# Kernel optimization log

Hardware: AMD Instinct MI355X
Metric: run time of the kernel (lower is better)

The kernel has to match this reference:

```python
import jax, jax.numpy as jnp
import numpy as np

N_NODE = 100000
HIDDEN = 128
BATCH = 4096
SESS_LEN = 50


def setup_inputs() -> dict:
    key = jax.random.key(0)
    k1, k2, k3, k4, k5 = jax.random.split(key, 5)
    return {
        "item_embedding": jax.random.normal(k1, (N_NODE, HIDDEN), dtype=jnp.float32),
        "items": jax.random.randint(k2, (BATCH, SESS_LEN), 0, N_NODE, dtype=jnp.int64),
        "A": jax.random.uniform(k3, (BATCH, BATCH), dtype=jnp.float32),
        "D": jax.random.uniform(k4, (BATCH, BATCH), dtype=jnp.float32),
        "target_embedding": jax.random.normal(k5, (BATCH, 1, 2 * HIDDEN), dtype=jnp.float32),
    }


def reference(item_embedding, items, A, D, target_embedding):
    # Gather per-session item embeddings: (batch, sess_len, hidden)
    seq_h = item_embedding[items]
    # Sum over session positions -> (batch, hidden)
    relation_emb = jnp.sum(seq_h, axis=1)
    # DA = D @ A, then propagate: (batch, batch) @ (batch, hidden)
    DA = jnp.matmul(D, A)
    relation_emb = jnp.matmul(DA, relation_emb)
    # Row-wise L2 normalization (torch.norm(dim=-1))
    norm = jnp.linalg.norm(relation_emb, axis=-1, keepdims=True)
    return relation_emb / norm
```

## Files before the change

### kernel.cpp

```cpp
#include <hip/hip_runtime.h>
#include <hip/hip_bf16.h>

#define BATCH   4096
#define HIDDEN  128
#define SESS    50
#define KTOT    4096
#define NB      ((size_t)BATCH * HIDDEN)

typedef __bf16 bf16x8 __attribute__((ext_vector_type(8)));
typedef float  f32x4  __attribute__((ext_vector_type(4)));
typedef float  f32x2  __attribute__((ext_vector_type(2)));

__device__ __forceinline__ f32x4 mfma_bf16(bf16x8 a, bf16x8 b, f32x4 c) {
    return __builtin_amdgcn_mfma_f32_16x16x32_bf16(a, b, c, 0, 0, 0);
}

__device__ __forceinline__ void gload16(const void* g, void* l) {
    __builtin_amdgcn_global_load_lds(
        (const __attribute__((address_space(1))) void*)g,
        (__attribute__((address_space(3))) void*)l, 16, 0, 0);
}


__global__ __launch_bounds__(256)
void gather_sum_kernel(const float* __restrict__ emb,
                       const int* __restrict__ items32,
                       __bf16* __restrict__ ETp) {
    __shared__ int sidx[4][SESS];
    const int t  = threadIdx.x;
    const int b0 = blockIdx.x * 4;
    const bool is64 = (items32[1] | items32[3] | items32[5] | items32[7] |
                       items32[9] | items32[11] | items32[13] | items32[15]) == 0;
    if (t < 4 * SESS) {
        const int w_ = t / SESS, s_ = t % SESS;
        sidx[w_][s_] = is64
            ? (int)((const long long*)items32)[(long)(b0 + w_) * SESS + s_]
            : items32[(b0 + w_) * SESS + s_];
    }
    __syncthreads();
    const int w    = t >> 6;
    const int lane = t & 63;
    const int c    = lane & 31;
    const int h    = lane >> 5;
    f32x4 acc = {0.f, 0.f, 0.f, 0.f};
#pragma unroll
    for (int i = 0; i < 25; ++i) {
        acc += *(const f32x4*)(emb + (long)sidx[w][h + 2 * i] * HIDDEN + c * 4);
    }
#pragma unroll
    for (int j = 0; j < 4; ++j) acc[j] += __shfl_xor(acc[j], 32, 64);
    if (h == 0) {
        const int b  = b0 + w;
        const int h0 = c * 4;
        const long pb = ((long)(b >> 3) << 10) + (b & 7) + ((h0 >> 4) << 7);
#pragma unroll
        for (int j = 0; j < 4; ++j)
            ETp[pb + ((h0 & 15) + j) * 8] = (__bf16)acc[j];
    }
}

__global__ __launch_bounds__(256, 2)
void gemm_mfma_kernel(const float* __restrict__ X,
                      const __bf16* __restrict__ Bpk,
                      float* __restrict__ Tp) {
    __shared__ __align__(16) float raw[16384];
    const int tid  = threadIdx.x;
    const int wave = tid >> 6;
    const int lane = tid & 63;
    const int lo   = lane & 15;
    const int quad = lane >> 4;
    const int rowBase = blockIdx.x * 16;
    const int sy      = blockIdx.y;
    const int kBase   = sy * 1024 + wave * 256;

    const float* apt   = X + (long)(rowBase + lo) * KTOT + kBase + quad * 8;
    const char*  bsrc  = (const char*)Bpk + ((long)(kBase >> 3) << 11);
    char*        sbase = (char*)raw + wave * 16384;

    f32x4 acc[8];
#pragma unroll
    for (int i = 0; i < 8; ++i) acc[i] = (f32x4){0.f, 0.f, 0.f, 0.f};

    f32x4 xa0[2], xa1[2];

#define STAGE(ks_, cur_) do {                                                \
    const char* g_ = bsrc + (ks_) * 8192 + lane * 16;                        \
    char* l_ = sbase + (cur_) * 8192;                                        \
    _Pragma("unroll")                                                        \
    for (int i_ = 0; i_ < 8; ++i_)                                           \
        gload16(g_ + i_ * 1024, l_ + i_ * 1024);                             \
} while (0)

    xa0[0] = *(const f32x4*)(apt);
    xa1[0] = *(const f32x4*)(apt + 4);
    STAGE(0, 0);
    xa0[1] = *(const f32x4*)(apt + 32);
    xa1[1] = *(const f32x4*)(apt + 36);
    STAGE(1, 1);

#define GITER(ks_, cur_, WAIT_, PRE_) do {                                   \
    asm volatile(WAIT_ ::: "memory");                                        \
    bf16x8 bb[8];                                                            \
    _Pragma("unroll")                                                        \
    for (int nt_ = 0; nt_ < 8; ++nt_)                                        \
        bb[nt_] = *(const bf16x8*)(sbase + (cur_) * 8192 + quad * 2048 +     \
                                   nt_ * 256 + lo * 16);                     \
    bf16x8 a;                                                                \
    a[0] = (__bf16)xa0[cur_][0]; a[1] = (__bf16)xa0[cur_][1];                \
    a[2] = (__bf16)xa0[cur_][2]; a[3] = (__bf16)xa0[cur_][3];                \
    a[4] = (__bf16)xa1[cur_][0]; a[5] = (__bf16)xa1[cur_][1];                \
    a[6] = (__bf16)xa1[cur_][2]; a[7] = (__bf16)xa1[cur_][3];                \
    asm volatile("s_waitcnt lgkmcnt(0)" ::: "memory");                       \
    __builtin_amdgcn_sched_barrier(0);                                       \
    if (PRE_) {                                                              \
        xa0[cur_] = *(const f32x4*)(apt + ((ks_) + 2) * 32);                 \
        xa1[cur_] = *(const f32x4*)(apt + ((ks_) + 2) * 32 + 4);             \
        STAGE((ks_) + 2, cur_);                                              \
    }                                                                        \
    _Pragma("unroll")                                                        \
    for (int nt_ = 0; nt_ < 8; ++nt_)                                        \
        acc[nt_] = mfma_bf16(a, bb[nt_], acc[nt_]);                          \
} while (0)

    GITER(0, 0, "s_waitcnt vmcnt(10)", 1);
    GITER(1, 1, "s_waitcnt vmcnt(10)", 1);
    GITER(2, 0, "s_waitcnt vmcnt(10)", 1);
    GITER(3, 1, "s_waitcnt vmcnt(10)", 1);
    GITER(4, 0, "s_waitcnt vmcnt(10)", 1);
    GITER(5, 1, "s_waitcnt vmcnt(10)", 1);
    GITER(6, 0, "s_waitcnt vmcnt(10)", 0);
    GITER(7, 1, "s_waitcnt vmcnt(0)",  0);

#undef GITER
#undef STAGE

    __syncthreads();
    float (*red)[16][132] = (float (*)[16][132])raw;
#pragma unroll
    for (int r = 0; r < 4; ++r) {
        const int dr = quad * 4 + r;
#pragma unroll
        for (int nt = 0; nt < 8; ++nt)
            red[wave][dr][nt * 16 + lo] = acc[nt][r];
    }
    __syncthreads();
    const int row = tid >> 4;
    const int cb  = (tid & 15) * 8;
    f32x4 v0 = {0.f, 0.f, 0.f, 0.f}, v1 = {0.f, 0.f, 0.f, 0.f};
#pragma unroll
    for (int w = 0; w < 4; ++w) {
        v0 += *(const f32x4*)&red[w][row][cb];
        v1 += *(const f32x4*)&red[w][row][cb + 4];
    }
    float* outp = Tp + (size_t)sy * NB + (long)(rowBase + row) * HIDDEN + cb;
    *(f32x4*)(outp)     = v0;
    *(f32x4*)(outp + 4) = v1;
}

__global__ __launch_bounds__(256)
void reduce4_kernel(const float* __restrict__ Tp, __bf16* __restrict__ TTp) {
    const size_t i = ((size_t)blockIdx.x * 256 + threadIdx.x) * 4;
    f32x4 a = *(const f32x4*)(Tp + i);
    a += *(const f32x4*)(Tp + NB + i);
    a += *(const f32x4*)(Tp + 2 * NB + i);
    a += *(const f32x4*)(Tp + 3 * NB + i);
    const int b  = (int)(i >> 7);
    const int h0 = (int)(i & 127);
    const long pb = ((long)(b >> 3) << 10) + (b & 7) + ((h0 >> 4) << 7);
#pragma unroll
    for (int j = 0; j < 4; ++j)
        TTp[pb + ((h0 & 15) + j) * 8] = (__bf16)a[j];
}

__global__ __launch_bounds__(256)
void reduce_norm_kernel(const float* __restrict__ Tp, float* __restrict__ out) {
    const int t    = threadIdx.x;
    const int w    = t >> 6;
    const int lane = t & 63;
    const int row  = blockIdx.x * 4 + w;
    const size_t base = (size_t)row * HIDDEN + lane * 2;
    f32x2 v = *(const f32x2*)(Tp + base);
    v += *(const f32x2*)(Tp + NB + base);
    v += *(const f32x2*)(Tp + 2 * NB + base);
    v += *(const f32x2*)(Tp + 3 * NB + base);
    float sq = v[0] * v[0] + v[1] * v[1];
#pragma unroll
    for (int m = 1; m < 64; m <<= 1) sq += __shfl_xor(sq, m, 64);
    const float s = rsqrtf(sq);
    f32x2 o = {v[0] * s, v[1] * s};
    *(f32x2*)(out + base) = o;
}

extern "C" void kernel_launch(void* const* d_in, const int* in_sizes, int n_in,
                              void* d_out, int out_size, void* d_ws, size_t ws_size,
                              hipStream_t stream) {
    const float* emb   = (const float*)d_in[0];
    const int*   items = (const int*)d_in[1];
    const float* A     = (const float*)d_in[2];
    const float* D     = (const float*)d_in[3];
    float* out = (float*)d_out;

    __bf16* ETp = (__bf16*)d_ws;
    __bf16* TTp = ETp + NB;
    float*  Tp  = (float*)(TTp + NB);

    gather_sum_kernel<<<BATCH / 4, 256, 0, stream>>>(emb, items, ETp);

    gemm_mfma_kernel<<<dim3(BATCH / 16, 4), 256, 0, stream>>>(A, ETp, Tp);
    reduce4_kernel<<<512, 256, 0, stream>>>(Tp, TTp);

    gemm_mfma_kernel<<<dim3(BATCH / 16, 4), 256, 0, stream>>>(D, TTp, Tp);
    reduce_norm_kernel<<<BATCH / 4, 256, 0, stream>>>(Tp, out);
}
```

Measured before the change: 229.4 us.

## Drop split-K in GEMMs and fuse reductions and normalization into epilogues

The GEMM kernel stops splitting K across four blocks and partial-sum buffers. Each block now walks the full K range, staging the fp32 X tile through double-buffered LDS with global-to-LDS loads and streaming B directly from global memory, with the N dimension split across waves. The bf16 repack for the second GEMM and the row L2 normalization move into the GEMM epilogues, which removes two reduction kernels and the fp32 partial-sum round trips. In exchange there are four times fewer blocks (256 blocks, one per CU), so latency hiding and parallelism drop, and B is no longer shared through LDS.

```diff
diff --git a/kernel.cpp b/kernel.cpp
--- a/kernel.cpp
+++ b/kernel.cpp
@@ -7,9 +7,15 @@
 #define KTOT    4096
 #define NB      ((size_t)BATCH * HIDDEN)
 
+#define BK        512
+#define KCH       16
+#define NTILES    (KTOT / BK)
+#define ROWSTRIDE 2064
+#define BUFSZ     (16 * ROWSTRIDE)
+
 typedef __bf16 bf16x8 __attribute__((ext_vector_type(8)));
+typedef __bf16 bf16x4 __attribute__((ext_vector_type(4)));
 typedef float  f32x4  __attribute__((ext_vector_type(4)));
-typedef float  f32x2  __attribute__((ext_vector_type(2)));
 
 __device__ __forceinline__ f32x4 mfma_bf16(bf16x8 a, bf16x8 b, f32x4 c) {
     return __builtin_amdgcn_mfma_f32_16x16x32_bf16(a, b, c, 0, 0, 0);
@@ -59,136 +65,115 @@
     }
 }
 
-__global__ __launch_bounds__(256, 2)
+template <int PHASE>
+__global__ __launch_bounds__(256, 1)
 void gemm_mfma_kernel(const float* __restrict__ X,
                       const __bf16* __restrict__ Bpk,
-                      float* __restrict__ Tp) {
-    __shared__ __align__(16) float raw[16384];
+                      __bf16* __restrict__ TTp,
+                      float* __restrict__ out) {
+    __shared__ __align__(16) char lds[2 * BUFSZ];
     const int tid  = threadIdx.x;
-    const int wave = tid >> 6;
+    const int w    = tid >> 6;
     const int lane = tid & 63;
     const int lo   = lane & 15;
     const int quad = lane >> 4;
     const int rowBase = blockIdx.x * 16;
-    const int sy      = blockIdx.y;
-    const int kBase   = sy * 1024 + wave * 256;
 
-    const float* apt   = X + (long)(rowBase + lo) * KTOT + kBase + quad * 8;
-    const char*  bsrc  = (const char*)Bpk + ((long)(kBase >> 3) << 11);
-    char*        sbase = (char*)raw + wave * 16384;
+    const float* xb = X + (size_t)(rowBase + 4 * w) * KTOT + lane * 4;
 
-    f32x4 acc[8];
-#pragma unroll
-    for (int i = 0; i < 8; ++i) acc[i] = (f32x4){0.f, 0.f, 0.f, 0.f};
-
-    f32x4 xa0[2], xa1[2];
-
-#define STAGE(ks_, cur_) do {                                                \
-    const char* g_ = bsrc + (ks_) * 8192 + lane * 16;                        \
-    char* l_ = sbase + (cur_) * 8192;                                        \
+#define STAGE(t_, b_) do {                                                   \
     _Pragma("unroll")                                                        \
-    for (int i_ = 0; i_ < 8; ++i_)                                           \
-        gload16(g_ + i_ * 1024, l_ + i_ * 1024);                             \
+    for (int r_ = 0; r_ < 4; ++r_) {                                         \
+        _Pragma("unroll")                                                    \
+        for (int p_ = 0; p_ < 2; ++p_) {                                     \
+            gload16(xb + (size_t)r_ * KTOT + (t_) * BK + p_ * 256,           \
+                    lds + (b_) * BUFSZ + (4 * w + r_) * ROWSTRIDE +          \
+                        p_ * 1024);                                          \
+        }                                                                    \
+    }                                                                        \
 } while (0)
 
-    xa0[0] = *(const f32x4*)(apt);
-    xa1[0] = *(const f32x4*)(apt + 4);
-    STAGE(0, 0);
-    xa0[1] = *(const f32x4*)(apt + 32);
-    xa1[1] = *(const f32x4*)(apt + 36);
-    STAGE(1, 1);
+    f32x4 acc0 = {0.f, 0.f, 0.f, 0.f};
+    f32x4 acc1 = {0.f, 0.f, 0.f, 0.f};
+    const __bf16* bq = Bpk + quad * 1024 + (2 * w) * 128 + lo * 8;
 
-#define GITER(ks_, cur_, WAIT_, PRE_) do {                                   \
-    asm volatile(WAIT_ ::: "memory");                                        \
-    bf16x8 bb[8];                                                            \
+#define KTILE(t_, cur_) do {                                                 \
+    const char* As = lds + (cur_) * BUFSZ + lo * ROWSTRIDE + quad * 32;      \
+    const __bf16* bp = bq + (size_t)(t_) * KCH * 4096;                       \
     _Pragma("unroll")                                                        \
-    for (int nt_ = 0; nt_ < 8; ++nt_)                                        \
-        bb[nt_] = *(const bf16x8*)(sbase + (cur_) * 8192 + quad * 2048 +     \
-                                   nt_ * 256 + lo * 16);                     \
-    bf16x8 a;                                                                \
-    a[0] = (__bf16)xa0[cur_][0]; a[1] = (__bf16)xa0[cur_][1];                \
-    a[2] = (__bf16)xa0[cur_][2]; a[3] = (__bf16)xa0[cur_][3];                \
-    a[4] = (__bf16)xa1[cur_][0]; a[5] = (__bf16)xa1[cur_][1];                \
-    a[6] = (__bf16)xa1[cur_][2]; a[7] = (__bf16)xa1[cur_][3];                \
-    asm volatile("s_waitcnt lgkmcnt(0)" ::: "memory");                       \
-    __builtin_amdgcn_sched_barrier(0);                                       \
-    if (PRE_) {                                                              \
-        xa0[cur_] = *(const f32x4*)(apt + ((ks_) + 2) * 32);                 \
-        xa1[cur_] = *(const f32x4*)(apt + ((ks_) + 2) * 32 + 4);             \
-        STAGE((ks_) + 2, cur_);                                              \
+    for (int ks = 0; ks < KCH; ++ks) {                                       \
+        const f32x4 a0 = *(const f32x4*)(As + ks * 128);                     \
+        const f32x4 a1 = *(const f32x4*)(As + ks * 128 + 16);                \
+        const bf16x8 b0 = *(const bf16x8*)(bp + (size_t)ks * 4096);          \
+        const bf16x8 b1 = *(const bf16x8*)(bp + (size_t)ks * 4096 + 128);    \
+        bf16x8 af;                                                           \
+        af[0] = (__bf16)a0[0]; af[1] = (__bf16)a0[1];                        \
+        af[2] = (__bf16)a0[2]; af[3] = (__bf16)a0[3];                        \
+        af[4] = (__bf16)a1[0]; af[5] = (__bf16)a1[1];                        \
+        af[6] = (__bf16)a1[2]; af[7] = (__bf16)a1[3];                        \
+        acc0 = mfma_bf16(af, b0, acc0);                                      \
+        acc1 = mfma_bf16(af, b1, acc1);                                      \
     }                                                                        \
-    _Pragma("unroll")                                                        \
-    for (int nt_ = 0; nt_ < 8; ++nt_)                                        \
-        acc[nt_] = mfma_bf16(a, bb[nt_], acc[nt_]);                          \
 } while (0)
 
-    GITER(0, 0, "s_waitcnt vmcnt(10)", 1);
-    GITER(1, 1, "s_waitcnt vmcnt(10)", 1);
-    GITER(2, 0, "s_waitcnt vmcnt(10)", 1);
-    GITER(3, 1, "s_waitcnt vmcnt(10)", 1);
-    GITER(4, 0, "s_waitcnt vmcnt(10)", 1);
-    GITER(5, 1, "s_waitcnt vmcnt(10)", 1);
-    GITER(6, 0, "s_waitcnt vmcnt(10)", 0);
-    GITER(7, 1, "s_waitcnt vmcnt(0)",  0);
-
-#undef GITER
+    STAGE(0, 0);
+    for (int t = 0; t < NTILES - 1; ++t) {
+        const int cur = t & 1;
+        STAGE(t + 1, cur ^ 1);
+        asm volatile("s_waitcnt vmcnt(8)" ::: "memory");
+        __builtin_amdgcn_s_barrier();
+        __builtin_amdgcn_sched_barrier(0);
+        KTILE(t, cur);
+        __builtin_amdgcn_s_barrier();
+        __builtin_amdgcn_sched_barrier(0);
+    }
+    {
+        asm volatile("s_waitcnt vmcnt(0)" ::: "memory");
+        __builtin_amdgcn_s_barrier();
+        __builtin_amdgcn_sched_barrier(0);
+        KTILE(NTILES - 1, (NTILES - 1) & 1);
+        __builtin_amdgcn_s_barrier();
+        __builtin_amdgcn_sched_barrier(0);
+    }
+#undef KTILE
 #undef STAGE
 
-    __syncthreads();
-    float (*red)[16][132] = (float (*)[16][132])raw;
+    if (PHASE == 1) {
+        __bf16* tb = TTp + ((rowBase >> 3) + (quad >> 1)) * 1024 + lo * 8 +
+                     (quad & 1) * 4;
+        bf16x4 p0, p1;
 #pragma unroll
-    for (int r = 0; r < 4; ++r) {
-        const int dr = quad * 4 + r;
+        for (int r = 0; r < 4; ++r) {
+            p0[r] = (__bf16)acc0[r];
+            p1[r] = (__bf16)acc1[r];
+        }
+        *(bf16x4*)(tb + (2 * w) * 128)     = p0;
+        *(bf16x4*)(tb + (2 * w + 1) * 128) = p1;
+    } else {
+        float (*Cs)[136] = (float (*)[136])lds;
 #pragma unroll
-        for (int nt = 0; nt < 8; ++nt)
-            red[wave][dr][nt * 16 + lo] = acc[nt][r];
+        for (int r = 0; r < 4; ++r) {
+            Cs[quad * 4 + r][(2 * w) * 16 + lo]     = acc0[r];
+            Cs[quad * 4 + r][(2 * w + 1) * 16 + lo] = acc1[r];
+        }
+        __syncthreads();
+        const int row = tid >> 4;
+        const int cg  = tid & 15;
+        const f32x4 c0 = *(const f32x4*)&Cs[row][cg * 8];
+        const f32x4 c1 = *(const f32x4*)&Cs[row][cg * 8 + 4];
+        float sq = c0[0] * c0[0] + c0[1] * c0[1] + c0[2] * c0[2] +
+                   c0[3] * c0[3] + c1[0] * c1[0] + c1[1] * c1[1] +
+                   c1[2] * c1[2] + c1[3] * c1[3];
+#pragma unroll
+        for (int m = 1; m < 16; m <<= 1) sq += __shfl_xor(sq, m, 64);
+        const float s = rsqrtf(sq);
+        float* op = out + (size_t)(rowBase + row) * HIDDEN + cg * 8;
+        f32x4 o0, o1;
+#pragma unroll
+        for (int j = 0; j < 4; ++j) { o0[j] = c0[j] * s; o1[j] = c1[j] * s; }
+        *(f32x4*)(op)     = o0;
+        *(f32x4*)(op + 4) = o1;
     }
-    __syncthreads();
-    const int row = tid >> 4;
-    const int cb  = (tid & 15) * 8;
-    f32x4 v0 = {0.f, 0.f, 0.f, 0.f}, v1 = {0.f, 0.f, 0.f, 0.f};
-#pragma unroll
-    for (int w = 0; w < 4; ++w) {
-        v0 += *(const f32x4*)&red[w][row][cb];
-        v1 += *(const f32x4*)&red[w][row][cb + 4];
-    }
-    float* outp = Tp + (size_t)sy * NB + (long)(rowBase + row) * HIDDEN + cb;
-    *(f32x4*)(outp)     = v0;
-    *(f32x4*)(outp + 4) = v1;
-}
-
-__global__ __launch_bounds__(256)
-void reduce4_kernel(const float* __restrict__ Tp, __bf16* __restrict__ TTp) {
-    const size_t i = ((size_t)blockIdx.x * 256 + threadIdx.x) * 4;
-    f32x4 a = *(const f32x4*)(Tp + i);
-    a += *(const f32x4*)(Tp + NB + i);
-    a += *(const f32x4*)(Tp + 2 * NB + i);
-    a += *(const f32x4*)(Tp + 3 * NB + i);
-    const int b  = (int)(i >> 7);
-    const int h0 = (int)(i & 127);
-    const long pb = ((long)(b >> 3) << 10) + (b & 7) + ((h0 >> 4) << 7);
-#pragma unroll
-    for (int j = 0; j < 4; ++j)
-        TTp[pb + ((h0 & 15) + j) * 8] = (__bf16)a[j];
-}
-
-__global__ __launch_bounds__(256)
-void reduce_norm_kernel(const float* __restrict__ Tp, float* __restrict__ out) {
-    const int t    = threadIdx.x;
-    const int w    = t >> 6;
-    const int lane = t & 63;
-    const int row  = blockIdx.x * 4 + w;
-    const size_t base = (size_t)row * HIDDEN + lane * 2;
-    f32x2 v = *(const f32x2*)(Tp + base);
-    v += *(const f32x2*)(Tp + NB + base);
-    v += *(const f32x2*)(Tp + 2 * NB + base);
-    v += *(const f32x2*)(Tp + 3 * NB + base);
-    float sq = v[0] * v[0] + v[1] * v[1];
-#pragma unroll
-    for (int m = 1; m < 64; m <<= 1) sq += __shfl_xor(sq, m, 64);
-    const float s = rsqrtf(sq);
-    f32x2 o = {v[0] * s, v[1] * s};
-    *(f32x2*)(out + base) = o;
 }
 
 extern "C" void kernel_launch(void* const* d_in, const int* in_sizes, int n_in,
@@ -202,13 +187,8 @@
 
     __bf16* ETp = (__bf16*)d_ws;
     __bf16* TTp = ETp + NB;
-    float*  Tp  = (float*)(TTp + NB);
 
     gather_sum_kernel<<<BATCH / 4, 256, 0, stream>>>(emb, items, ETp);
-
-    gemm_mfma_kernel<<<dim3(BATCH / 16, 4), 256, 0, stream>>>(A, ETp, Tp);
-    reduce4_kernel<<<512, 256, 0, stream>>>(Tp, TTp);
-
-    gemm_mfma_kernel<<<dim3(BATCH / 16, 4), 256, 0, stream>>>(D, TTp, Tp);
-    reduce_norm_kernel<<<BATCH / 4, 256, 0, stream>>>(Tp, out);
+    gemm_mfma_kernel<1><<<BATCH / 16, 256, 0, stream>>>(A, ETp, TTp, nullptr);
+    gemm_mfma_kernel<2><<<BATCH / 16, 256, 0, stream>>>(D, TTp, nullptr, out);
 }
```

New measurement: 227.0 us. Within noise of the previous version (-1.1%).
